# Kernel optimization log

Measured on AMD Instinct MI355X. Metric: run time of the kernel, lower is better.

Reference implementation:

```python
import jax, jax.numpy as jnp
import numpy as np
import math

# PIM parameters (match init_kwargs)
WL_W = 8          # weight bit width
WL_A = 8          # activation bit width
CELLBIT = 2       # bits per memristor cell
SUBARRAY = 128    # crossbar column size
ADC = 5           # ADC precision bits
ONOFF = 10.0      # on/off conductance ratio
VARI = 0.05       # state-dependent variation std
SAF_PROP = 0.001  # stuck-at-fault probability
STRIDE = 1
PAD = 1


def adc_quant(x, bit):
    # LinearQuantizeOut: uniform quantization between global min/max to 2^bit levels
    mn = jnp.min(x)
    delta = jnp.max(x) - mn
    step = delta * (2.0 ** (-bit))
    step = jnp.where(step <= 0, 1.0, step)
    idx = jnp.clip(jnp.floor((x - mn) / step), 0.0, 2.0 ** bit - 1.0)
    return idx * step + mn


def _forward(x, weight, bias):
    N, C, H, W = x.shape
    out_ch, _, kh, kw = weight.shape
    # im2col (channel-major patch ordering, same as torch.nn.Unfold)
    patches = jax.lax.conv_general_dilated_patches(
        x, (kh, kw), (STRIDE, STRIDE), ((PAD, PAD), (PAD, PAD)))  # [N, C*kh*kw, Ho, Wo]
    _, L, Ho, Wo = patches.shape
    inp = patches.reshape(N, L, Ho * Wo).transpose(0, 2, 1).reshape(-1, L)  # [rows, L]
    wflat = weight.reshape(out_ch, L)

    cellRange = 2 ** CELLBIT
    n_cells = WL_W // CELLBIT - 1   # loop count as in original (drops top cell)
    n_abits = WL_A - 1
    lower = 1.0 / ONOFF

    # activation quantization, per-tensor (qa_tensor)
    a_levels = 2.0 ** (WL_A - 1) - 1.0
    a_scale = jnp.maximum(jnp.max(inp), 1e-8) / a_levels
    inputQ = jnp.round(inp / a_scale)

    # pad columns to a multiple of SUBARRAY
    numSub = math.ceil(L / SUBARRAY)
    padn = numSub * SUBARRAY - L
    inputQ = jnp.pad(inputQ, ((0, 0), (0, padn))).reshape(-1, numSub, SUBARRAY)
    wpad = jnp.pad(wflat, ((0, 0), (0, padn))).reshape(out_ch, numSub, SUBARRAY)

    # weight quantization per (out_channel, subarray) group (qw_tensor)
    w_levels = 2.0 ** (WL_W - 1) - 1.0
    w_scale = jnp.maximum(jnp.max(jnp.abs(wpad), axis=-1, keepdims=True), 1e-8) / w_levels  # [out, numSub, 1]
    wq = jnp.round(wpad / w_scale)  # signed ints in [-w_levels, w_levels]

    # randomness: SAF masks fixed per cell level k (apply_SAF, done once);
    # state-dependent noise drawn fresh for every (z, k) iteration as in forward()
    kmask, knoise = jax.random.split(jax.random.key(42))
    probs = jax.random.uniform(kmask, (n_cells,) + wq.shape)
    sa0 = probs < SAF_PROP
    sa1 = probs > 1.0 - SAF_PROP
    noise = jax.random.normal(knoise, (n_abits, n_cells) + wq.shape) * VARI

    rows = inputQ.shape[0]
    output = jnp.zeros((rows, out_ch), dtype=x.dtype)
    ws_T = w_scale[:, :, 0].T[:, None, :]  # [numSub, 1, out]

    for z in range(n_abits):
        inputB = jnp.fmod(inputQ, 2.0)
        inputQ = jnp.round((inputQ - inputB) / 2.0)
        Xd = wq
        outD = jnp.zeros((rows, out_ch), dtype=x.dtype)
        for k in range(n_cells):
            rem = jnp.fmod(Xd, float(cellRange))
            Xd = jnp.round((Xd - rem) / cellRange)
            rQ = rem + rem * noise[z, k]          # state_dependent variation
            rQ = jnp.where(sa0[k], lower, rQ)      # stuck-at-0 -> low conductance
            rQ = jnp.where(sa1[k], jnp.sign(rQ), rQ)  # stuck-at-1 -> full conductance
            # [numSub, rows, sub] x [numSub, sub, out] -> [numSub, rows, out]
            partial = jnp.einsum('srk,sko->sro', inputB.transpose(1, 0, 2), rQ.transpose(1, 2, 0))
            pq = (adc_quant(partial, ADC) * ws_T).sum(0)  # [rows, out]
            outD = outD + pq * float(cellRange ** k)
        output = output + outD * (2.0 ** z) * a_scale

    out = output.reshape(N, Ho, Wo, out_ch).transpose(0, 3, 1, 2)
    return out + bias[None, :, None, None]


def setup_inputs() -> dict:
    key = jax.random.key(0)
    k1, k2, k3 = jax.random.split(key, 3)
    x = jax.random.uniform(k1, (8, 64, 32, 32), dtype=jnp.float32)  # post-ReLU-like activations
    weight = jax.random.normal(k2, (128, 64, 3, 3), dtype=jnp.float32) * 0.05
    bias = jax.random.normal(k3, (128,), dtype=jnp.float32) * 0.01
    return {"x": x, "weight": weight, "bias": bias}


def reference(x, weight, bias):
    return _forward(x, weight, bias)
```

## Files before the change

kernel.cpp:

```cpp
#include <hip/hip_runtime.h>
#include <stdint.h>

#define FPOFF _Pragma("clang fp contract(off)")

#define ROWS 8192
#define OC 128
#define NS 5
#define SUB 128
#define LP 640
#define LREAL 576
#define NZ 7
#define NK 3
#define NSLOT 21
#define NPTOT 245760
#define NNTOT 1720320

#define OFF_HDR      0u
#define OFF_WSCALE   256u
#define OFF_WQ       4096u
#define OFF_CLS      86016u
#define OFF_INPUTQ   331776u
#define OFF_PACKB    5574656u
#define OFF_RQ       10162176u
#define OFF_PART0    17043456u
#define OFF_PART1    38014976u
#define OFF_PART2    58986496u
#define OFF_OUTACC   79958016u

struct U2 { uint32_t x, y; };

__host__ __device__ static inline uint32_t rotl32(uint32_t v, int d){ return (v << d) | (v >> (32 - d)); }

__host__ __device__ static inline U2 threefry(uint32_t k0, uint32_t k1, uint32_t c0, uint32_t c1){
  uint32_t ks2 = k0 ^ k1 ^ 0x1BD11BDAu;
  uint32_t x0 = c0 + k0, x1 = c1 + k1;
#define TFR(r) { x0 += x1; x1 = rotl32(x1, r); x1 ^= x0; }
  TFR(13) TFR(15) TFR(26) TFR(6)  x0 += k1;  x1 += ks2 + 1u;
  TFR(17) TFR(29) TFR(16) TFR(24) x0 += ks2; x1 += k0 + 2u;
  TFR(13) TFR(15) TFR(26) TFR(6)  x0 += k0;  x1 += k1 + 3u;
  TFR(17) TFR(29) TFR(16) TFR(24) x0 += k1;  x1 += ks2 + 4u;
  TFR(13) TFR(15) TFR(26) TFR(6)  x0 += ks2; x1 += k0 + 5u;
#undef TFR
  U2 r; r.x = x0; r.y = x1; return r;
}

__device__ static inline float u2f(uint32_t b){
  return __uint_as_float((b >> 9) | 0x3F800000u) - 1.0f;
}

__device__ static inline uint32_t encf(float f){
  uint32_t u = __float_as_uint(f);
  return (u & 0x80000000u) ? ~u : (u | 0x80000000u);
}
__device__ static inline float decf(uint32_t e){
  return (e & 0x80000000u) ? __uint_as_float(e & 0x7FFFFFFFu) : __uint_as_float(~e);
}

__device__ static inline float xla_erfinv(float x){
  FPOFF
  float m = x * x;
  float w = -(float)log1p((double)(-m));
  float p;
  if (w < 5.0f){
    w = w - 2.5f;
    p = 2.81022636e-08f;
    p = 3.43273939e-07f  + p * w;
    p = -3.5233877e-06f  + p * w;
    p = -4.39150654e-06f + p * w;
    p = 0.00021858087f   + p * w;
    p = -0.00125372503f  + p * w;
    p = -0.00417768164f  + p * w;
    p = 0.246640727f     + p * w;
    p = 1.50140941f      + p * w;
  } else {
    w = (float)sqrt((double)w) - 3.0f;
    p = -0.000200214257f;
    p = 0.000100950558f  + p * w;
    p = 0.00134934322f   + p * w;
    p = -0.00367342844f  + p * w;
    p = 0.00573950773f   + p * w;
    p = -0.0076224613f   + p * w;
    p = 0.00943887047f   + p * w;
    p = 1.00167406f      + p * w;
    p = 2.83297682f      + p * w;
  }
  return p * x;
}


__global__ void k_init(uint32_t* hdr){
  int t = threadIdx.x;
  if (t == 0) hdr[0] = 0u;
  if (t < NSLOT){ hdr[8 + t] = 0xFFFFFFFFu; hdr[32 + t] = 0u; }
}

__global__ void k_xmax(const float* __restrict__ x, uint32_t* hdr){
  __shared__ float red[4];
  int t = threadIdx.x;
  const float4* x4 = (const float4*)x;
  int base = blockIdx.x * 1024 + t;
  float m = 0.0f;
#pragma unroll
  for (int i = 0; i < 4; ++i){
    float4 v = x4[base + i * 256];
    m = fmaxf(m, fmaxf(fmaxf(v.x, v.y), fmaxf(v.z, v.w)));
  }
  for (int off = 32; off; off >>= 1) m = fmaxf(m, __shfl_down(m, off));
  if ((t & 63) == 0) red[t >> 6] = m;
  __syncthreads();
  if (t == 0){
    m = fmaxf(fmaxf(red[0], red[1]), fmaxf(red[2], red[3]));
    atomicMax(&hdr[0], encf(m));
  }
}

__global__ void k_wq(const float* __restrict__ wt, float* __restrict__ wscale, int8_t* __restrict__ wq){
  FPOFF
  int s = blockIdx.x, o = blockIdx.y, t = threadIdx.x;
  int l0 = s * SUB + t, l1 = l0 + 64;
  float w0 = (l0 < LREAL) ? wt[o * LREAL + l0] : 0.f;
  float w1 = (l1 < LREAL) ? wt[o * LREAL + l1] : 0.f;
  float m = fmaxf(fabsf(w0), fabsf(w1));
  for (int off = 32; off; off >>= 1) m = fmaxf(m, __shfl_down(m, off));
  m = __shfl(m, 0);
  float ws = fmaxf(m, 1e-8f) / 127.0f;
  if (t == 0) wscale[s * OC + o] = ws;
  wq[o * LP + l0] = (int8_t)(int)rintf(w0 / ws);
  wq[o * LP + l1] = (int8_t)(int)rintf(w1 / ws);
}

__global__ void k_inputq(const float* __restrict__ x, const uint32_t* __restrict__ hdr, uint8_t* __restrict__ iq){
  FPOFF
  int r = blockIdx.x, t = threadIdx.x;
  float a_scale = fmaxf(decf(hdr[0]), 1e-8f) / 127.0f;
  int n = r >> 10, hw = r & 1023, oh = hw >> 5, ow = hw & 31;
  for (int l = t; l < LP; l += 256){
    float val = 0.f;
    if (l < LREAL){
      int c = l / 9, r9 = l - c * 9, ki = r9 / 3, kj = r9 - ki * 3;
      int ih = oh - 1 + ki, iw = ow - 1 + kj;
      if ((unsigned)ih < 32u && (unsigned)iw < 32u)
        val = x[(((n << 6) + c) << 10) + (ih << 5) + iw];
    }
    iq[r * LP + l] = (uint8_t)(int)rintf(val / a_scale);
  }
}

__global__ void k_pack(const uint8_t* __restrict__ iq, uint32_t* __restrict__ packB){
  int gid = blockIdx.x * 256 + threadIdx.x;
  if (gid >= ROWS * 20) return;
  int r = gid / 20, sw = gid - r * 20;
  const uint4* p4 = (const uint4*)(iq + r * LP + sw * 32);
  uint4 a = p4[0], b2 = p4[1];
  uint32_t wds[8] = {a.x, a.y, a.z, a.w, b2.x, b2.y, b2.z, b2.w};
  uint32_t out[NZ];
#pragma unroll
  for (int z = 0; z < NZ; ++z) out[z] = 0u;
#pragma unroll
  for (int tt = 0; tt < 32; ++tt){
    uint32_t byte = (wds[tt >> 2] >> ((tt & 3) * 8)) & 0xFFu;
#pragma unroll
    for (int z = 0; z < NZ; ++z) out[z] |= ((byte >> z) & 1u) << tt;
  }
#pragma unroll
  for (int z = 0; z < NZ; ++z) packB[(z * ROWS + r) * 20 + sw] = out[z];
}

__global__ void k_cls(uint8_t* __restrict__ cls, uint32_t km0, uint32_t km1){
  int i = blockIdx.x * 256 + threadIdx.x;
  if (i >= NPTOT) return;
  U2 r = threefry(km0, km1, 0u, (uint32_t)i);
  float f = u2f(r.x ^ r.y);
  cls[i] = (f < 0.001f) ? 1 : ((f > 0.999f) ? 2 : 0);
}

__global__ void k_rq(const int8_t* __restrict__ wq, const uint8_t* __restrict__ cls,
                     float* __restrict__ rq, uint32_t kn0, uint32_t kn1){
  FPOFF
  int i = blockIdx.x * 256 + threadIdx.x;
  if (i >= NNTOT) return;
  U2 rr = threefry(kn0, kn1, 0u, (uint32_t)i);
  uint32_t bits = rr.x ^ rr.y;
  int j = i & 127;
  int t = i >> 7;
  int s = t % 5;
  int t2 = t / 5;
  int o = t2 & 127;
  int t3 = t2 >> 7;
  int k = t3 % 3;
  int z = t3 / 3;
  float f = u2f(bits);
  float u = fmaxf(-0x1.fffffep-1f, f * 2.0f + (-0x1.fffffep-1f));
  float nv = (0x1.6a09e6p+0f * xla_erfinv(u)) * 0.05f;
  int wv = (int)wq[o * LP + s * SUB + j];
  int r0 = wv % 4;  int x1 = (wv - r0) / 4;
  int r1 = x1 % 4;  int x2 = (x1 - r1) / 4;
  int r2 = x2 % 4;
  int rem = (k == 0) ? r0 : ((k == 1) ? r1 : r2);
  float remf = (float)rem;
  float v = remf + remf * nv;
  int c = cls[((k * OC + o) * NS + s) * SUB + j];
  if (c == 1) v = 0.1f;
  else if (c == 2) v = (v > 0.f) ? 1.f : ((v < 0.f) ? -1.f : 0.f);
  rq[(((z * NK + k) * NS + s) * SUB + j) * OC + o] = v;
}

__global__ __launch_bounds__(256) void k_mm(const float* __restrict__ rq_slice,
                                            const uint32_t* __restrict__ packB_z,
                                            float* __restrict__ partial,
                                            uint32_t* __restrict__ hdr, int slot){
  FPOFF
  __shared__ float lrq[128 * 32];
  __shared__ float red[8];
  const int tid  = threadIdx.x;
  const int wave = tid >> 6;
  const int lane = tid & 63;
  const int s    = blockIdx.z;
  const int r0   = blockIdx.x * 128 + lane;
  const int OB   = blockIdx.y * 32;
  const int o0   = OB + wave * 8;

  {
    const float* gsrc = rq_slice + (size_t)s * SUB * OC + OB;
#pragma unroll
    for (int it = 0; it < 4; ++it){
      const int f = it * 256 + tid;
      const int j = f >> 3, q = f & 7;
      const float4 v = *(const float4*)(gsrc + (size_t)j * OC + q * 4);
      *(float4*)&lrq[j * 32 + q * 4] = v;
    }
  }

  const uint4 bwa4 = *(const uint4*)(packB_z + (size_t)r0 * 20 + s * 4);
  const uint4 bwb4 = *(const uint4*)(packB_z + (size_t)(r0 + 64) * 20 + s * 4);
  const uint32_t bwa[4] = {bwa4.x, bwa4.y, bwa4.z, bwa4.w};
  const uint32_t bwb[4] = {bwb4.x, bwb4.y, bwb4.z, bwb4.w};

  __syncthreads();

  float acc0[8], acc1[8];
#pragma unroll
  for (int i = 0; i < 8; ++i){ acc0[i] = 0.f; acc1[i] = 0.f; }

#pragma unroll
  for (int w = 0; w < 4; ++w){
    const uint32_t ba = bwa[w], bb = bwb[w];
#pragma unroll
    for (int jj = 0; jj < 32; ++jj){
      const int mska = ((int)(ba << (31 - jj))) >> 31;
      const int mskb = ((int)(bb << (31 - jj))) >> 31;
      const float bfa = __uint_as_float((uint32_t)mska & 0x3F800000u);
      const float bfb = __uint_as_float((uint32_t)mskb & 0x3F800000u);
      const float* lp = &lrq[(w * 32 + jj) * 32 + wave * 8];
#pragma unroll
      for (int i = 0; i < 8; ++i){
        const float rv = lp[i];
        acc0[i] = __builtin_fmaf(rv, bfa, acc0[i]);
        acc1[i] = __builtin_fmaf(rv, bfb, acc1[i]);
      }
    }
  }

  {
    float4* p0 = (float4*)(partial + (size_t)(s * ROWS + r0) * OC + o0);
    p0[0] = make_float4(acc0[0], acc0[1], acc0[2], acc0[3]);
    p0[1] = make_float4(acc0[4], acc0[5], acc0[6], acc0[7]);
    float4* p1 = (float4*)(partial + (size_t)(s * ROWS + r0 + 64) * OC + o0);
    p1[0] = make_float4(acc1[0], acc1[1], acc1[2], acc1[3]);
    p1[1] = make_float4(acc1[4], acc1[5], acc1[6], acc1[7]);
  }

  float mn = acc0[0], mx = acc0[0];
#pragma unroll
  for (int i = 1; i < 8; ++i){ mn = fminf(mn, acc0[i]); mx = fmaxf(mx, acc0[i]); }
#pragma unroll
  for (int i = 0; i < 8; ++i){ mn = fminf(mn, acc1[i]); mx = fmaxf(mx, acc1[i]); }
  for (int off = 32; off; off >>= 1){
    mn = fminf(mn, __shfl_down(mn, off));
    mx = fmaxf(mx, __shfl_down(mx, off));
  }
  if (lane == 0){ red[wave] = mn; red[4 + wave] = mx; }
  __syncthreads();
  if (tid == 0){
    mn = fminf(fminf(red[0], red[1]), fminf(red[2], red[3]));
    mx = fmaxf(fmaxf(red[4], red[5]), fmaxf(red[6], red[7]));
    atomicMin(&hdr[8 + slot], encf(mn));
    atomicMax(&hdr[32 + slot], encf(mx));
  }
}

__global__ void k_quantz(const float* __restrict__ p0, const float* __restrict__ p1,
                         const float* __restrict__ p2, const float* __restrict__ wscale,
                         const uint32_t* __restrict__ hdr, float* __restrict__ outacc,
                         float* __restrict__ out, const float* __restrict__ bias, int z){
  FPOFF
  int e = blockIdx.x * 256 + threadIdx.x;
  int r = e >> 7, o = e & 127;
  float pqk[NK];
#pragma unroll
  for (int k = 0; k < NK; ++k){
    const float* part = (k == 0) ? p0 : ((k == 1) ? p1 : p2);
    float mn = decf(hdr[8 + z * NK + k]);
    float mx = decf(hdr[32 + z * NK + k]);
    float step = (mx - mn) * 0.03125f;
    if (!(step > 0.f)) step = 1.0f;
    float pq = 0.f;
#pragma unroll
    for (int s = 0; s < NS; ++s){
      float v = part[(size_t)(s * ROWS + r) * OC + o];
      float fidx = floorf((v - mn) / step);
      fidx = fminf(fmaxf(fidx, 0.f), 31.f);
      float qv = fidx * step + mn;
      pq = pq + qv * wscale[s * OC + o];
    }
    pqk[k] = pq;
  }
  float outD = pqk[0] + pqk[1] * 4.0f;
  float tt = outD + pqk[2] * 16.0f;
  float a_scale = fmaxf(decf(hdr[0]), 1e-8f) / 127.0f;
  float contrib = (tt * (float)(1 << z)) * a_scale;
  if (z == 0) outacc[e] = contrib;
  else if (z < NZ - 1) outacc[e] = outacc[e] + contrib;
  else {
    float res = outacc[e] + contrib;
    int n = r >> 10, hw = r & 1023;
    out[(((n << 7) + o) << 10) + hw] = res + bias[o];
  }
}

extern "C" void kernel_launch(void* const* d_in, const int* in_sizes, int n_in,
                              void* d_out, int out_size, void* d_ws, size_t ws_size,
                              hipStream_t stream){
  const float* x    = (const float*)d_in[0];
  const float* wt   = (const float*)d_in[1];
  const float* bias = (const float*)d_in[2];
  float* out = (float*)d_out;
  char* ws = (char*)d_ws;
  uint32_t* hdr    = (uint32_t*)(ws + OFF_HDR);
  float*    wscale = (float*)(ws + OFF_WSCALE);
  int8_t*   wq     = (int8_t*)(ws + OFF_WQ);
  uint8_t*  cls    = (uint8_t*)(ws + OFF_CLS);
  uint8_t*  iq     = (uint8_t*)(ws + OFF_INPUTQ);
  uint32_t* packB  = (uint32_t*)(ws + OFF_PACKB);
  float*    rq     = (float*)(ws + OFF_RQ);
  float*    part[3] = { (float*)(ws + OFF_PART0), (float*)(ws + OFF_PART1),
                        (float*)(ws + OFF_PART2) };
  float*    outacc = (float*)(ws + OFF_OUTACC);

  U2 p0 = threefry(0u, 42u, 0u, 0u);
  U2 p1 = threefry(0u, 42u, 0u, 1u);
  uint32_t km0 = p0.x, km1 = p0.y, kn0 = p1.x, kn1 = p1.y;

  hipLaunchKernelGGL(k_init,   dim3(1),           dim3(64),  0, stream, hdr);
  hipLaunchKernelGGL(k_xmax,   dim3(128),         dim3(256), 0, stream, x, hdr);
  hipLaunchKernelGGL(k_wq,     dim3(5, 128),      dim3(64),  0, stream, wt, wscale, wq);
  hipLaunchKernelGGL(k_inputq, dim3(8192),        dim3(256), 0, stream, x, hdr, iq);
  hipLaunchKernelGGL(k_pack,   dim3(640),         dim3(256), 0, stream, iq, packB);
  hipLaunchKernelGGL(k_cls,    dim3(NPTOT / 256), dim3(256), 0, stream, cls, km0, km1);
  hipLaunchKernelGGL(k_rq,     dim3(NNTOT / 256), dim3(256), 0, stream, wq, cls, rq, kn0, kn1);

  for (int z = 0; z < NZ; ++z){
    const uint32_t* pbz = packB + (size_t)z * ROWS * 20;
    for (int k = 0; k < NK; ++k){
      int slot = z * NK + k;
      const float* rqsl = rq + (size_t)slot * NS * SUB * OC;
      hipLaunchKernelGGL(k_mm, dim3(64, 4, 5), dim3(256), 0, stream,
                         rqsl, pbz, part[k], hdr, slot);
    }
    hipLaunchKernelGGL(k_quantz, dim3(4096), dim3(256), 0, stream,
                       part[0], part[1], part[2], wscale, hdr, outacc, out, bias, z);
  }
}
```

Before: 728.2 us.

## Merge per-k matmul launches and overlap previous-z quantization in one kernel

Replaces the three per-k matmul launches per activation bit with a single launch covering all k and subarrays. The same grid also runs the ADC quantization and accumulation of the previous bit plane, using double-buffered partial sums, and a final quantize pass handles the last plane. This cuts launch count and lets the memory-bound quantize work overlap with compute. The cost is a doubled partial workspace and a branch-divergent fused kernel whose two block types compete for resources.

Measured after the change: 593.1 us. 18.6% less time.

```diff
diff --git a/kernel.cpp b/kernel.cpp
--- a/kernel.cpp
+++ b/kernel.cpp
@@ -14,6 +14,7 @@
 #define NSLOT 21
 #define NPTOT 245760
 #define NNTOT 1720320
+#define PARTSZ 5242880
 
 #define OFF_HDR      0u
 #define OFF_WSCALE   256u
@@ -22,10 +23,8 @@
 #define OFF_INPUTQ   331776u
 #define OFF_PACKB    5574656u
 #define OFF_RQ       10162176u
-#define OFF_PART0    17043456u
-#define OFF_PART1    38014976u
-#define OFF_PART2    58986496u
-#define OFF_OUTACC   79958016u
+#define OFF_PARTS    17043456u
+#define OFF_OUTACC   142872576u
 
 struct U2 { uint32_t x, y; };
 
@@ -205,87 +204,127 @@
   rq[(((z * NK + k) * NS + s) * SUB + j) * OC + o] = v;
 }
 
-__global__ __launch_bounds__(256) void k_mm(const float* __restrict__ rq_slice,
-                                            const uint32_t* __restrict__ packB_z,
-                                            float* __restrict__ partial,
-                                            uint32_t* __restrict__ hdr, int slot){
-  FPOFF
-  __shared__ float lrq[128 * 32];
-  __shared__ float red[8];
-  const int tid  = threadIdx.x;
-  const int wave = tid >> 6;
-  const int lane = tid & 63;
-  const int s    = blockIdx.z;
-  const int r0   = blockIdx.x * 128 + lane;
-  const int OB   = blockIdx.y * 32;
-  const int o0   = OB + wave * 8;
-
-  {
-    const float* gsrc = rq_slice + (size_t)s * SUB * OC + OB;
-#pragma unroll
-    for (int it = 0; it < 4; ++it){
-      const int f = it * 256 + tid;
-      const int j = f >> 3, q = f & 7;
-      const float4 v = *(const float4*)(gsrc + (size_t)j * OC + q * 4);
-      *(float4*)&lrq[j * 32 + q * 4] = v;
-    }
-  }
-
-  const uint4 bwa4 = *(const uint4*)(packB_z + (size_t)r0 * 20 + s * 4);
-  const uint4 bwb4 = *(const uint4*)(packB_z + (size_t)(r0 + 64) * 20 + s * 4);
-  const uint32_t bwa[4] = {bwa4.x, bwa4.y, bwa4.z, bwa4.w};
-  const uint32_t bwb[4] = {bwb4.x, bwb4.y, bwb4.z, bwb4.w};
-
-  __syncthreads();
-
-  float acc0[8], acc1[8];
-#pragma unroll
-  for (int i = 0; i < 8; ++i){ acc0[i] = 0.f; acc1[i] = 0.f; }
-
-#pragma unroll
-  for (int w = 0; w < 4; ++w){
-    const uint32_t ba = bwa[w], bb = bwb[w];
-#pragma unroll
-    for (int jj = 0; jj < 32; ++jj){
-      const int mska = ((int)(ba << (31 - jj))) >> 31;
-      const int mskb = ((int)(bb << (31 - jj))) >> 31;
-      const float bfa = __uint_as_float((uint32_t)mska & 0x3F800000u);
-      const float bfb = __uint_as_float((uint32_t)mskb & 0x3F800000u);
-      const float* lp = &lrq[(w * 32 + jj) * 32 + wave * 8];
-#pragma unroll
-      for (int i = 0; i < 8; ++i){
-        const float rv = lp[i];
-        acc0[i] = __builtin_fmaf(rv, bfa, acc0[i]);
-        acc1[i] = __builtin_fmaf(rv, bfb, acc1[i]);
+__global__ __launch_bounds__(256) void k_mmq(
+    const float* __restrict__ rq_z, const uint32_t* __restrict__ packB_z,
+    float* __restrict__ partCur, const float* __restrict__ partPrev,
+    const float* __restrict__ wscale, uint32_t* __restrict__ hdr,
+    float* __restrict__ outacc, float* __restrict__ out,
+    const float* __restrict__ bias, int z)
+{
+  FPOFF
+  const int bz = blockIdx.z;
+  if (bz < 15){
+    __shared__ float lrq[128 * 32];
+    __shared__ float red[8];
+    const int tid  = threadIdx.x;
+    const int wave = tid >> 6;
+    const int lane = tid & 63;
+    const int k    = bz / 5;
+    const int s    = bz - k * 5;
+    const int slot = z * NK + k;
+    const float* rq_slice = rq_z + (size_t)k * (NS * SUB * OC);
+    float* partial = partCur + (size_t)k * PARTSZ;
+    const int r0   = blockIdx.x * 128 + lane;
+    const int OB   = blockIdx.y * 32;
+    const int o0   = OB + wave * 8;
+
+    {
+      const float* gsrc = rq_slice + (size_t)s * SUB * OC + OB;
+#pragma unroll
+      for (int it = 0; it < 4; ++it){
+        const int f = it * 256 + tid;
+        const int j = f >> 3, q = f & 7;
+        const float4 v = *(const float4*)(gsrc + (size_t)j * OC + q * 4);
+        *(float4*)&lrq[j * 32 + q * 4] = v;
       }
     }
-  }
-
-  {
-    float4* p0 = (float4*)(partial + (size_t)(s * ROWS + r0) * OC + o0);
-    p0[0] = make_float4(acc0[0], acc0[1], acc0[2], acc0[3]);
-    p0[1] = make_float4(acc0[4], acc0[5], acc0[6], acc0[7]);
-    float4* p1 = (float4*)(partial + (size_t)(s * ROWS + r0 + 64) * OC + o0);
-    p1[0] = make_float4(acc1[0], acc1[1], acc1[2], acc1[3]);
-    p1[1] = make_float4(acc1[4], acc1[5], acc1[6], acc1[7]);
-  }
-
-  float mn = acc0[0], mx = acc0[0];
-#pragma unroll
-  for (int i = 1; i < 8; ++i){ mn = fminf(mn, acc0[i]); mx = fmaxf(mx, acc0[i]); }
-#pragma unroll
-  for (int i = 0; i < 8; ++i){ mn = fminf(mn, acc1[i]); mx = fmaxf(mx, acc1[i]); }
-  for (int off = 32; off; off >>= 1){
-    mn = fminf(mn, __shfl_down(mn, off));
-    mx = fmaxf(mx, __shfl_down(mx, off));
-  }
-  if (lane == 0){ red[wave] = mn; red[4 + wave] = mx; }
-  __syncthreads();
-  if (tid == 0){
-    mn = fminf(fminf(red[0], red[1]), fminf(red[2], red[3]));
-    mx = fmaxf(fmaxf(red[4], red[5]), fmaxf(red[6], red[7]));
-    atomicMin(&hdr[8 + slot], encf(mn));
-    atomicMax(&hdr[32 + slot], encf(mx));
+
+    const uint4 bwa4 = *(const uint4*)(packB_z + (size_t)r0 * 20 + s * 4);
+    const uint4 bwb4 = *(const uint4*)(packB_z + (size_t)(r0 + 64) * 20 + s * 4);
+    const uint32_t bwa[4] = {bwa4.x, bwa4.y, bwa4.z, bwa4.w};
+    const uint32_t bwb[4] = {bwb4.x, bwb4.y, bwb4.z, bwb4.w};
+
+    __syncthreads();
+
+    float acc0[8], acc1[8];
+#pragma unroll
+    for (int i = 0; i < 8; ++i){ acc0[i] = 0.f; acc1[i] = 0.f; }
+
+#pragma unroll
+    for (int w = 0; w < 4; ++w){
+      const uint32_t ba = bwa[w], bb = bwb[w];
+#pragma unroll
+      for (int jj = 0; jj < 32; ++jj){
+        const int mska = ((int)(ba << (31 - jj))) >> 31;
+        const int mskb = ((int)(bb << (31 - jj))) >> 31;
+        const float bfa = __uint_as_float((uint32_t)mska & 0x3F800000u);
+        const float bfb = __uint_as_float((uint32_t)mskb & 0x3F800000u);
+        const float* lp = &lrq[(w * 32 + jj) * 32 + wave * 8];
+#pragma unroll
+        for (int i = 0; i < 8; ++i){
+          const float rv = lp[i];
+          acc0[i] = __builtin_fmaf(rv, bfa, acc0[i]);
+          acc1[i] = __builtin_fmaf(rv, bfb, acc1[i]);
+        }
+      }
+    }
+
+    {
+      float4* p0 = (float4*)(partial + (size_t)(s * ROWS + r0) * OC + o0);
+      p0[0] = make_float4(acc0[0], acc0[1], acc0[2], acc0[3]);
+      p0[1] = make_float4(acc0[4], acc0[5], acc0[6], acc0[7]);
+      float4* p1 = (float4*)(partial + (size_t)(s * ROWS + r0 + 64) * OC + o0);
+      p1[0] = make_float4(acc1[0], acc1[1], acc1[2], acc1[3]);
+      p1[1] = make_float4(acc1[4], acc1[5], acc1[6], acc1[7]);
+    }
+
+    float mn = acc0[0], mx = acc0[0];
+#pragma unroll
+    for (int i = 1; i < 8; ++i){ mn = fminf(mn, acc0[i]); mx = fmaxf(mx, acc0[i]); }
+#pragma unroll
+    for (int i = 0; i < 8; ++i){ mn = fminf(mn, acc1[i]); mx = fmaxf(mx, acc1[i]); }
+    for (int off = 32; off; off >>= 1){
+      mn = fminf(mn, __shfl_down(mn, off));
+      mx = fmaxf(mx, __shfl_down(mx, off));
+    }
+    if (lane == 0){ red[wave] = mn; red[4 + wave] = mx; }
+    __syncthreads();
+    if (tid == 0){
+      mn = fminf(fminf(red[0], red[1]), fminf(red[2], red[3]));
+      mx = fmaxf(fmaxf(red[4], red[5]), fmaxf(red[6], red[7]));
+      atomicMin(&hdr[8 + slot], encf(mn));
+      atomicMax(&hdr[32 + slot], encf(mx));
+    }
+  } else {
+    const int zP = z - 1;
+    const int qid = (bz - 15) * 256 + blockIdx.y * 64 + blockIdx.x;
+    const int e = qid * 256 + threadIdx.x;
+    const int r = e >> 7, o = e & 127;
+    float pqk[NK];
+#pragma unroll
+    for (int k = 0; k < NK; ++k){
+      const float* part = partPrev + (size_t)k * PARTSZ;
+      float mn = decf(hdr[8 + zP * NK + k]);
+      float mx = decf(hdr[32 + zP * NK + k]);
+      float step = (mx - mn) * 0.03125f;
+      if (!(step > 0.f)) step = 1.0f;
+      float pq = 0.f;
+#pragma unroll
+      for (int s = 0; s < NS; ++s){
+        float v = part[(size_t)(s * ROWS + r) * OC + o];
+        float fidx = floorf((v - mn) / step);
+        fidx = fminf(fmaxf(fidx, 0.f), 31.f);
+        float qv = fidx * step + mn;
+        pq = pq + qv * wscale[s * OC + o];
+      }
+      pqk[k] = pq;
+    }
+    float outD = pqk[0] + pqk[1] * 4.0f;
+    float tt = outD + pqk[2] * 16.0f;
+    float a_scale = fmaxf(decf(hdr[0]), 1e-8f) / 127.0f;
+    float contrib = (tt * (float)(1 << zP)) * a_scale;
+    if (zP == 0) outacc[e] = contrib;
+    else outacc[e] = outacc[e] + contrib;
   }
 }
 
@@ -343,8 +382,7 @@
   uint8_t*  iq     = (uint8_t*)(ws + OFF_INPUTQ);
   uint32_t* packB  = (uint32_t*)(ws + OFF_PACKB);
   float*    rq     = (float*)(ws + OFF_RQ);
-  float*    part[3] = { (float*)(ws + OFF_PART0), (float*)(ws + OFF_PART1),
-                        (float*)(ws + OFF_PART2) };
+  float*    parts  = (float*)(ws + OFF_PARTS);
   float*    outacc = (float*)(ws + OFF_OUTACC);
 
   U2 p0 = threefry(0u, 42u, 0u, 0u);
@@ -360,14 +398,15 @@
   hipLaunchKernelGGL(k_rq,     dim3(NNTOT / 256), dim3(256), 0, stream, wq, cls, rq, kn0, kn1);
 
   for (int z = 0; z < NZ; ++z){
+    float*       cur  = parts + (size_t)((z & 1) ? 3 : 0) * PARTSZ;
+    const float* prev = parts + (size_t)((z & 1) ? 0 : 3) * PARTSZ;
+    const float* rqz  = rq + (size_t)z * NK * NS * SUB * OC;
     const uint32_t* pbz = packB + (size_t)z * ROWS * 20;
-    for (int k = 0; k < NK; ++k){
-      int slot = z * NK + k;
-      const float* rqsl = rq + (size_t)slot * NS * SUB * OC;
-      hipLaunchKernelGGL(k_mm, dim3(64, 4, 5), dim3(256), 0, stream,
-                         rqsl, pbz, part[k], hdr, slot);
-    }
-    hipLaunchKernelGGL(k_quantz, dim3(4096), dim3(256), 0, stream,
-                       part[0], part[1], part[2], wscale, hdr, outacc, out, bias, z);
-  }
-}
+    dim3 grid(64, 4, (z == 0) ? 15 : 31);
+    hipLaunchKernelGGL(k_mmq, grid, dim3(256), 0, stream,
+                       rqz, pbz, cur, prev, wscale, hdr, outacc, out, bias, z);
+  }
+  hipLaunchKernelGGL(k_quantz, dim3(4096), dim3(256), 0, stream,
+                     parts, parts + PARTSZ, parts + 2 * (size_t)PARTSZ,
+                     wscale, hdr, outacc, out, bias, 6);
+}
```
